# Kernel optimization log

Hardware: AMD Instinct MI355X
Metric: run time of the kernel (lower is better)

## Reference

```python
import jax, jax.numpy as jnp
import numpy as np

B, D, N_TYPES = 512, 768, 16
MARGIN = 1.0


def setup_inputs() -> dict:
    key = jax.random.key(0)
    k1, k2 = jax.random.split(key)
    entity_types = jax.random.randint(k1, (B,), 0, N_TYPES, dtype=jnp.int64)
    embeddings = jax.random.normal(k2, (B, D), dtype=jnp.float32)
    return {"entity_types": entity_types, "embeddings": embeddings}


def _pairwise_l2(x):
    # Euclidean distance matrix [B, B], matching torch.cdist(x, x, p=2)
    sq_norm = jnp.sum(x * x, axis=-1)  # [B]
    sq = sq_norm[:, None] + sq_norm[None, :] - 2.0 * (x @ x.T)
    sq = jnp.maximum(sq, 0.0)
    # safe sqrt: zero gradient where sq == 0 (diagonal)
    return jnp.where(sq > 0, jnp.sqrt(jnp.where(sq > 0, sq, 1.0)), 0.0)


def reference(entity_types, embeddings):
    # type_coherence[i, j] = (type_i == type_j)
    type_coherence = entity_types[:, None] == entity_types[None, :]  # [B, B]
    # valid_triplets[a, p, n] = same_type(a, p) & different_type(a, n)
    valid_triplets = type_coherence[:, :, None] & (~type_coherence)[:, None, :]  # [B, B, B]
    distances = _pairwise_l2(embeddings)  # [B, B]
    # triplet_distances[a, p, n] = (d[a, p] - d[a, n]) masked by validity
    triplet_distances = (distances[:, :, None] - distances[:, None, :]) * valid_triplets
    # NOTE: faithful to original — margin added to ALL B^3 entries before clamp,
    # so each invalid triplet contributes clamp(margin, 0) = margin to the sum.
    loss = jnp.sum(jnp.maximum(triplet_distances + MARGIN, 0.0))
    return loss / jnp.sum(valid_triplets)
```

## Files before the change

kernel.cpp:

```cpp
#include <hip/hip_runtime.h>

#define BSZ 512
#define DIM 768
#define KSPLIT 4
#define KSEG (DIM / KSPLIT)
#define KT 32
#define NCHK (KSEG / KT)
#define TILE 64
#define NTYPES 16
#define MARGIN 1.0f

__global__ __launch_bounds__(256) void dot_partial_kernel(
    const float* __restrict__ emb,
    float* __restrict__ part,
    float* __restrict__ ndiag,
    double* __restrict__ accum)
{
    const int tid = threadIdx.x;
    const int tx = tid & 15, ty = tid >> 4;
    const int blk = blockIdx.x;
    const int ks = blk >> 6;
    const int tile = blk & 63;
    const int ti = tile >> 3, tj = tile & 7;
    const int i0 = ti * TILE, j0 = tj * TILE;

    if (blk == 0 && tid == 0) *accum = 0.0;

    __shared__ float sA[2][KT][TILE + 4];
    __shared__ float sB[2][KT][TILE + 4];

    const int srow = tid >> 2;
    const int g = tid & 3;
    const float* gA = emb + (size_t)(i0 + srow) * DIM + ks * KSEG;
    const float* gB = emb + (size_t)(j0 + srow) * DIM + ks * KSEG;

    float4 a0 = *(const float4*)(gA + 4 * g);
    float4 a1 = *(const float4*)(gA + 4 * (g + 4));
    float4 b0 = *(const float4*)(gB + 4 * g);
    float4 b1 = *(const float4*)(gB + 4 * (g + 4));

    {
        float (*pA)[TILE + 4] = sA[0];
        float (*pB)[TILE + 4] = sB[0];
        pA[4*g+0][srow]=a0.x; pA[4*g+1][srow]=a0.y; pA[4*g+2][srow]=a0.z; pA[4*g+3][srow]=a0.w;
        pA[4*(g+4)+0][srow]=a1.x; pA[4*(g+4)+1][srow]=a1.y; pA[4*(g+4)+2][srow]=a1.z; pA[4*(g+4)+3][srow]=a1.w;
        pB[4*g+0][srow]=b0.x; pB[4*g+1][srow]=b0.y; pB[4*g+2][srow]=b0.z; pB[4*g+3][srow]=b0.w;
        pB[4*(g+4)+0][srow]=b1.x; pB[4*(g+4)+1][srow]=b1.y; pB[4*(g+4)+2][srow]=b1.z; pB[4*(g+4)+3][srow]=b1.w;
    }
    __syncthreads();

    float acc[4][4] = {};

    for (int c = 0; c < NCHK; ++c) {
        const int cur = c & 1;
        float4 qa0, qa1, qb0, qb1;
        if (c + 1 < NCHK) {
            const float* pa = gA + (c + 1) * KT;
            const float* pb = gB + (c + 1) * KT;
            qa0 = *(const float4*)(pa + 4 * g);
            qa1 = *(const float4*)(pa + 4 * (g + 4));
            qb0 = *(const float4*)(pb + 4 * g);
            qb1 = *(const float4*)(pb + 4 * (g + 4));
        }
        #pragma unroll
        for (int k = 0; k < KT; ++k) {
            float4 av = *(const float4*)&sA[cur][k][4 * ty];
            float4 bv = *(const float4*)&sB[cur][k][4 * tx];
            acc[0][0] = fmaf(av.x, bv.x, acc[0][0]);
            acc[0][1] = fmaf(av.x, bv.y, acc[0][1]);
            acc[0][2] = fmaf(av.x, bv.z, acc[0][2]);
            acc[0][3] = fmaf(av.x, bv.w, acc[0][3]);
            acc[1][0] = fmaf(av.y, bv.x, acc[1][0]);
            acc[1][1] = fmaf(av.y, bv.y, acc[1][1]);
            acc[1][2] = fmaf(av.y, bv.z, acc[1][2]);
            acc[1][3] = fmaf(av.y, bv.w, acc[1][3]);
            acc[2][0] = fmaf(av.z, bv.x, acc[2][0]);
            acc[2][1] = fmaf(av.z, bv.y, acc[2][1]);
            acc[2][2] = fmaf(av.z, bv.z, acc[2][2]);
            acc[2][3] = fmaf(av.z, bv.w, acc[2][3]);
            acc[3][0] = fmaf(av.w, bv.x, acc[3][0]);
            acc[3][1] = fmaf(av.w, bv.y, acc[3][1]);
            acc[3][2] = fmaf(av.w, bv.z, acc[3][2]);
            acc[3][3] = fmaf(av.w, bv.w, acc[3][3]);
        }
        if (c + 1 < NCHK) {
            float (*pA)[TILE + 4] = sA[1 - cur];
            float (*pB)[TILE + 4] = sB[1 - cur];
            pA[4*g+0][srow]=qa0.x; pA[4*g+1][srow]=qa0.y; pA[4*g+2][srow]=qa0.z; pA[4*g+3][srow]=qa0.w;
            pA[4*(g+4)+0][srow]=qa1.x; pA[4*(g+4)+1][srow]=qa1.y; pA[4*(g+4)+2][srow]=qa1.z; pA[4*(g+4)+3][srow]=qa1.w;
            pB[4*g+0][srow]=qb0.x; pB[4*g+1][srow]=qb0.y; pB[4*g+2][srow]=qb0.z; pB[4*g+3][srow]=qb0.w;
            pB[4*(g+4)+0][srow]=qb1.x; pB[4*(g+4)+1][srow]=qb1.y; pB[4*(g+4)+2][srow]=qb1.z; pB[4*(g+4)+3][srow]=qb1.w;
        }
        __syncthreads();
    }

    float* pbuf = part + (size_t)ks * BSZ * BSZ;
    #pragma unroll
    for (int r = 0; r < 4; ++r) {
        const int gi = i0 + 4 * ty + r;
        float4 v = make_float4(acc[r][0], acc[r][1], acc[r][2], acc[r][3]);
        *(float4*)&pbuf[(size_t)gi * BSZ + j0 + 4 * tx] = v;
    }
    if (ti == tj && tx == ty) {
        #pragma unroll
        for (int r = 0; r < 4; ++r)
            ndiag[ks * BSZ + i0 + 4 * ty + r] = acc[r][r];
    }
}

__global__ __launch_bounds__(256) void triplet_kernel(
    const float* __restrict__ part, const float* __restrict__ ndiag,
    const int* __restrict__ types, double* __restrict__ accum)
{
    const int a = blockIdx.x;
    const int tid = threadIdx.x;
    const int lane = tid & 63;
    __shared__ float nrm[BSZ];
    __shared__ float pos[BSZ], neg[BSZ];
    __shared__ int npos, nneg;
    __shared__ float wsum[4];
    if (tid == 0) { npos = 0; nneg = 0; }
    for (int j = tid; j < BSZ; j += 256)
        nrm[j] = ndiag[j] + ndiag[BSZ + j] + ndiag[2 * BSZ + j] + ndiag[3 * BSZ + j];
    const int ta = types[a];
    __syncthreads();

    const float na = nrm[a];
    const size_t rb = (size_t)a * BSZ;
    const size_t PS = (size_t)BSZ * BSZ;

    for (int j = tid; j < BSZ; j += 256) {
        const float sp = part[rb + j] + part[PS + rb + j]
                       + part[2 * PS + rb + j] + part[3 * PS + rb + j];
        const float d = sqrtf(fmaxf(na + nrm[j] - 2.f * sp, 0.f));
        const bool isp = (types[j] == ta);
        const unsigned long long m = __ballot(isp);
        const unsigned long long below = m & ((1ull << lane) - 1ull);
        const int cp = __popcll(m);
        int basep = 0, basen = 0;
        if (lane == 0) {
            basep = atomicAdd(&npos, cp);
            basen = atomicAdd(&nneg, 64 - cp);
        }
        basep = __shfl(basep, 0);
        basen = __shfl(basen, 0);
        const int pbelow = (int)__popcll(below);
        if (isp) pos[basep + pbelow] = d;
        else     neg[basen + (lane - pbelow)] = d;
    }
    __syncthreads();
    const int np = npos, nn = nneg;

    float local = 0.f;
    for (int pi = 0; pi < np; ++pi) {
        const float dpm = pos[pi] + MARGIN;
        for (int n = tid; n < nn; n += 256)
            local += fmaxf(dpm - neg[n], 0.f);
    }

    #pragma unroll
    for (int off = 32; off > 0; off >>= 1) local += __shfl_down(local, off);
    if (lane == 0) wsum[tid >> 6] = local;
    __syncthreads();
    if (tid == 0) {
        double s = (double)wsum[0] + (double)wsum[1] + (double)wsum[2] + (double)wsum[3];
        atomicAdd(accum, s);
    }
}

__global__ void finalize_kernel(const int* __restrict__ types,
                                const double* __restrict__ accum,
                                float* __restrict__ out) {
    __shared__ int cnt[NTYPES];
    if (threadIdx.x < NTYPES) cnt[threadIdx.x] = 0;
    __syncthreads();
    for (int i = threadIdx.x; i < BSZ; i += blockDim.x) atomicAdd(&cnt[types[i]], 1);
    __syncthreads();
    if (threadIdx.x == 0) {
        long long V = 0;
        for (int t = 0; t < NTYPES; t++) {
            long long c = cnt[t];
            V += c * c * (long long)(BSZ - c);
        }
        const long long B3 = (long long)BSZ * BSZ * BSZ;
        double total = *accum + (double)(B3 - V) * (double)MARGIN;
        out[0] = (float)(total / (double)V);
    }
}

extern "C" void kernel_launch(void* const* d_in, const int* in_sizes, int n_in,
                              void* d_out, int out_size, void* d_ws, size_t ws_size,
                              hipStream_t stream) {
    const int* types = (const int*)d_in[0];
    const float* emb = (const float*)d_in[1];
    float* out = (float*)d_out;

    float* part = (float*)d_ws;
    float* ndiag = part + (size_t)KSPLIT * BSZ * BSZ;
    double* accum = (double*)(ndiag + KSPLIT * BSZ);

    dot_partial_kernel<<<256, 256, 0, stream>>>(emb, part, ndiag, accum);
    triplet_kernel<<<BSZ, 256, 0, stream>>>(part, ndiag, types, accum);
    finalize_kernel<<<1, 256, 0, stream>>>(types, accum, out);
}
```

Baseline: 80.33 us.

## Fuse GEMM, triplet and finalize kernels into one persistent kernel with grid barrier

Merges the three launches into a single 256-block kernel. A spin-wait atomic grid barrier separates the partial-dot GEMM phase from the triplet phase, and each block now handles two anchors. A last-block-done counter runs the finalize step in place of a separate kernel. This removes two launch gaps but adds a memset, halves the parallelism in the triplet phase, and relies on all 256 blocks being co-resident for the barrier.

```diff
diff --git a/kernel.cpp b/kernel.cpp
--- a/kernel.cpp
+++ b/kernel.cpp
@@ -9,12 +9,15 @@
 #define TILE 64
 #define NTYPES 16
 #define MARGIN 1.0f
-
-__global__ __launch_bounds__(256) void dot_partial_kernel(
-    const float* __restrict__ emb,
+#define NBLK 256
+
+__global__ __launch_bounds__(256) void fused_kernel(
+    const float* __restrict__ emb, const int* __restrict__ types,
     float* __restrict__ part,
     float* __restrict__ ndiag,
-    double* __restrict__ accum)
+    double* __restrict__ accum,
+    unsigned* __restrict__ ctrl,
+    float* __restrict__ out)
 {
     const int tid = threadIdx.x;
     const int tx = tid & 15, ty = tid >> 4;
@@ -24,167 +27,183 @@
     const int ti = tile >> 3, tj = tile & 7;
     const int i0 = ti * TILE, j0 = tj * TILE;
 
-    if (blk == 0 && tid == 0) *accum = 0.0;
-
     __shared__ float sA[2][KT][TILE + 4];
     __shared__ float sB[2][KT][TILE + 4];
-
-    const int srow = tid >> 2;
-    const int g = tid & 3;
-    const float* gA = emb + (size_t)(i0 + srow) * DIM + ks * KSEG;
-    const float* gB = emb + (size_t)(j0 + srow) * DIM + ks * KSEG;
-
-    float4 a0 = *(const float4*)(gA + 4 * g);
-    float4 a1 = *(const float4*)(gA + 4 * (g + 4));
-    float4 b0 = *(const float4*)(gB + 4 * g);
-    float4 b1 = *(const float4*)(gB + 4 * (g + 4));
-
-    {
-        float (*pA)[TILE + 4] = sA[0];
-        float (*pB)[TILE + 4] = sB[0];
-        pA[4*g+0][srow]=a0.x; pA[4*g+1][srow]=a0.y; pA[4*g+2][srow]=a0.z; pA[4*g+3][srow]=a0.w;
-        pA[4*(g+4)+0][srow]=a1.x; pA[4*(g+4)+1][srow]=a1.y; pA[4*(g+4)+2][srow]=a1.z; pA[4*(g+4)+3][srow]=a1.w;
-        pB[4*g+0][srow]=b0.x; pB[4*g+1][srow]=b0.y; pB[4*g+2][srow]=b0.z; pB[4*g+3][srow]=b0.w;
-        pB[4*(g+4)+0][srow]=b1.x; pB[4*(g+4)+1][srow]=b1.y; pB[4*(g+4)+2][srow]=b1.z; pB[4*(g+4)+3][srow]=b1.w;
-    }
-    __syncthreads();
-
-    float acc[4][4] = {};
-
-    for (int c = 0; c < NCHK; ++c) {
-        const int cur = c & 1;
-        float4 qa0, qa1, qb0, qb1;
-        if (c + 1 < NCHK) {
-            const float* pa = gA + (c + 1) * KT;
-            const float* pb = gB + (c + 1) * KT;
-            qa0 = *(const float4*)(pa + 4 * g);
-            qa1 = *(const float4*)(pa + 4 * (g + 4));
-            qb0 = *(const float4*)(pb + 4 * g);
-            qb1 = *(const float4*)(pb + 4 * (g + 4));
-        }
-        #pragma unroll
-        for (int k = 0; k < KT; ++k) {
-            float4 av = *(const float4*)&sA[cur][k][4 * ty];
-            float4 bv = *(const float4*)&sB[cur][k][4 * tx];
-            acc[0][0] = fmaf(av.x, bv.x, acc[0][0]);
-            acc[0][1] = fmaf(av.x, bv.y, acc[0][1]);
-            acc[0][2] = fmaf(av.x, bv.z, acc[0][2]);
-            acc[0][3] = fmaf(av.x, bv.w, acc[0][3]);
-            acc[1][0] = fmaf(av.y, bv.x, acc[1][0]);
-            acc[1][1] = fmaf(av.y, bv.y, acc[1][1]);
-            acc[1][2] = fmaf(av.y, bv.z, acc[1][2]);
-            acc[1][3] = fmaf(av.y, bv.w, acc[1][3]);
-            acc[2][0] = fmaf(av.z, bv.x, acc[2][0]);
-            acc[2][1] = fmaf(av.z, bv.y, acc[2][1]);
-            acc[2][2] = fmaf(av.z, bv.z, acc[2][2]);
-            acc[2][3] = fmaf(av.z, bv.w, acc[2][3]);
-            acc[3][0] = fmaf(av.w, bv.x, acc[3][0]);
-            acc[3][1] = fmaf(av.w, bv.y, acc[3][1]);
-            acc[3][2] = fmaf(av.w, bv.z, acc[3][2]);
-            acc[3][3] = fmaf(av.w, bv.w, acc[3][3]);
-        }
-        if (c + 1 < NCHK) {
-            float (*pA)[TILE + 4] = sA[1 - cur];
-            float (*pB)[TILE + 4] = sB[1 - cur];
-            pA[4*g+0][srow]=qa0.x; pA[4*g+1][srow]=qa0.y; pA[4*g+2][srow]=qa0.z; pA[4*g+3][srow]=qa0.w;
-            pA[4*(g+4)+0][srow]=qa1.x; pA[4*(g+4)+1][srow]=qa1.y; pA[4*(g+4)+2][srow]=qa1.z; pA[4*(g+4)+3][srow]=qa1.w;
-            pB[4*g+0][srow]=qb0.x; pB[4*g+1][srow]=qb0.y; pB[4*g+2][srow]=qb0.z; pB[4*g+3][srow]=qb0.w;
-            pB[4*(g+4)+0][srow]=qb1.x; pB[4*(g+4)+1][srow]=qb1.y; pB[4*(g+4)+2][srow]=qb1.z; pB[4*(g+4)+3][srow]=qb1.w;
-        }
-        __syncthreads();
-    }
-
-    float* pbuf = part + (size_t)ks * BSZ * BSZ;
-    #pragma unroll
-    for (int r = 0; r < 4; ++r) {
-        const int gi = i0 + 4 * ty + r;
-        float4 v = make_float4(acc[r][0], acc[r][1], acc[r][2], acc[r][3]);
-        *(float4*)&pbuf[(size_t)gi * BSZ + j0 + 4 * tx] = v;
-    }
-    if (ti == tj && tx == ty) {
-        #pragma unroll
-        for (int r = 0; r < 4; ++r)
-            ndiag[ks * BSZ + i0 + 4 * ty + r] = acc[r][r];
-    }
-}
-
-__global__ __launch_bounds__(256) void triplet_kernel(
-    const float* __restrict__ part, const float* __restrict__ ndiag,
-    const int* __restrict__ types, double* __restrict__ accum)
-{
-    const int a = blockIdx.x;
-    const int tid = threadIdx.x;
-    const int lane = tid & 63;
     __shared__ float nrm[BSZ];
     __shared__ float pos[BSZ], neg[BSZ];
     __shared__ int npos, nneg;
     __shared__ float wsum[4];
-    if (tid == 0) { npos = 0; nneg = 0; }
+    __shared__ int winner;
+    __shared__ int cnt[NTYPES];
+
+    {
+        const int srow = tid >> 2;
+        const int g = tid & 3;
+        const float* gA = emb + (size_t)(i0 + srow) * DIM + ks * KSEG;
+        const float* gB = emb + (size_t)(j0 + srow) * DIM + ks * KSEG;
+
+        float4 a0 = *(const float4*)(gA + 4 * g);
+        float4 a1 = *(const float4*)(gA + 4 * (g + 4));
+        float4 b0 = *(const float4*)(gB + 4 * g);
+        float4 b1 = *(const float4*)(gB + 4 * (g + 4));
+        {
+            float (*pA)[TILE + 4] = sA[0];
+            float (*pB)[TILE + 4] = sB[0];
+            pA[4*g+0][srow]=a0.x; pA[4*g+1][srow]=a0.y; pA[4*g+2][srow]=a0.z; pA[4*g+3][srow]=a0.w;
+            pA[4*(g+4)+0][srow]=a1.x; pA[4*(g+4)+1][srow]=a1.y; pA[4*(g+4)+2][srow]=a1.z; pA[4*(g+4)+3][srow]=a1.w;
+            pB[4*g+0][srow]=b0.x; pB[4*g+1][srow]=b0.y; pB[4*g+2][srow]=b0.z; pB[4*g+3][srow]=b0.w;
+            pB[4*(g+4)+0][srow]=b1.x; pB[4*(g+4)+1][srow]=b1.y; pB[4*(g+4)+2][srow]=b1.z; pB[4*(g+4)+3][srow]=b1.w;
+        }
+        __syncthreads();
+
+        float acc[4][4] = {};
+        for (int c = 0; c < NCHK; ++c) {
+            const int cur = c & 1;
+            float4 qa0, qa1, qb0, qb1;
+            if (c + 1 < NCHK) {
+                const float* pa = gA + (c + 1) * KT;
+                const float* pb = gB + (c + 1) * KT;
+                qa0 = *(const float4*)(pa + 4 * g);
+                qa1 = *(const float4*)(pa + 4 * (g + 4));
+                qb0 = *(const float4*)(pb + 4 * g);
+                qb1 = *(const float4*)(pb + 4 * (g + 4));
+            }
+            #pragma unroll
+            for (int k = 0; k < KT; ++k) {
+                float4 av = *(const float4*)&sA[cur][k][4 * ty];
+                float4 bv = *(const float4*)&sB[cur][k][4 * tx];
+                acc[0][0] = fmaf(av.x, bv.x, acc[0][0]);
+                acc[0][1] = fmaf(av.x, bv.y, acc[0][1]);
+                acc[0][2] = fmaf(av.x, bv.z, acc[0][2]);
+                acc[0][3] = fmaf(av.x, bv.w, acc[0][3]);
+                acc[1][0] = fmaf(av.y, bv.x, acc[1][0]);
+                acc[1][1] = fmaf(av.y, bv.y, acc[1][1]);
+                acc[1][2] = fmaf(av.y, bv.z, acc[1][2]);
+                acc[1][3] = fmaf(av.y, bv.w, acc[1][3]);
+                acc[2][0] = fmaf(av.z, bv.x, acc[2][0]);
+                acc[2][1] = fmaf(av.z, bv.y, acc[2][1]);
+                acc[2][2] = fmaf(av.z, bv.z, acc[2][2]);
+                acc[2][3] = fmaf(av.z, bv.w, acc[2][3]);
+                acc[3][0] = fmaf(av.w, bv.x, acc[3][0]);
+                acc[3][1] = fmaf(av.w, bv.y, acc[3][1]);
+                acc[3][2] = fmaf(av.w, bv.z, acc[3][2]);
+                acc[3][3] = fmaf(av.w, bv.w, acc[3][3]);
+            }
+            if (c + 1 < NCHK) {
+                float (*pA)[TILE + 4] = sA[1 - cur];
+                float (*pB)[TILE + 4] = sB[1 - cur];
+                pA[4*g+0][srow]=qa0.x; pA[4*g+1][srow]=qa0.y; pA[4*g+2][srow]=qa0.z; pA[4*g+3][srow]=qa0.w;
+                pA[4*(g+4)+0][srow]=qa1.x; pA[4*(g+4)+1][srow]=qa1.y; pA[4*(g+4)+2][srow]=qa1.z; pA[4*(g+4)+3][srow]=qa1.w;
+                pB[4*g+0][srow]=qb0.x; pB[4*g+1][srow]=qb0.y; pB[4*g+2][srow]=qb0.z; pB[4*g+3][srow]=qb0.w;
+                pB[4*(g+4)+0][srow]=qb1.x; pB[4*(g+4)+1][srow]=qb1.y; pB[4*(g+4)+2][srow]=qb1.z; pB[4*(g+4)+3][srow]=qb1.w;
+            }
+            __syncthreads();
+        }
+
+        float* pbuf = part + (size_t)ks * BSZ * BSZ;
+        #pragma unroll
+        for (int r = 0; r < 4; ++r) {
+            const int gi = i0 + 4 * ty + r;
+            float4 v = make_float4(acc[r][0], acc[r][1], acc[r][2], acc[r][3]);
+            *(float4*)&pbuf[(size_t)gi * BSZ + j0 + 4 * tx] = v;
+        }
+        if (ti == tj && tx == ty) {
+            #pragma unroll
+            for (int r = 0; r < 4; ++r)
+                ndiag[ks * BSZ + i0 + 4 * ty + r] = acc[r][r];
+        }
+    }
+
+    __syncthreads();
+    if (tid == 0) {
+        __hip_atomic_fetch_add(&ctrl[0], 1u, __ATOMIC_RELEASE,
+                               __HIP_MEMORY_SCOPE_AGENT);
+        while (__hip_atomic_load(&ctrl[0], __ATOMIC_RELAXED,
+                                 __HIP_MEMORY_SCOPE_AGENT) < NBLK)
+            __builtin_amdgcn_s_sleep(2);
+        (void)__hip_atomic_load(&ctrl[0], __ATOMIC_ACQUIRE,
+                                __HIP_MEMORY_SCOPE_AGENT);
+    }
+    __syncthreads();
+
+    const int lane = tid & 63;
     for (int j = tid; j < BSZ; j += 256)
         nrm[j] = ndiag[j] + ndiag[BSZ + j] + ndiag[2 * BSZ + j] + ndiag[3 * BSZ + j];
-    const int ta = types[a];
-    __syncthreads();
-
-    const float na = nrm[a];
-    const size_t rb = (size_t)a * BSZ;
+    __syncthreads();
+
     const size_t PS = (size_t)BSZ * BSZ;
-
-    for (int j = tid; j < BSZ; j += 256) {
-        const float sp = part[rb + j] + part[PS + rb + j]
-                       + part[2 * PS + rb + j] + part[3 * PS + rb + j];
-        const float d = sqrtf(fmaxf(na + nrm[j] - 2.f * sp, 0.f));
-        const bool isp = (types[j] == ta);
-        const unsigned long long m = __ballot(isp);
-        const unsigned long long below = m & ((1ull << lane) - 1ull);
-        const int cp = __popcll(m);
-        int basep = 0, basen = 0;
-        if (lane == 0) {
-            basep = atomicAdd(&npos, cp);
-            basen = atomicAdd(&nneg, 64 - cp);
-        }
-        basep = __shfl(basep, 0);
-        basen = __shfl(basen, 0);
-        const int pbelow = (int)__popcll(below);
-        if (isp) pos[basep + pbelow] = d;
-        else     neg[basen + (lane - pbelow)] = d;
-    }
-    __syncthreads();
-    const int np = npos, nn = nneg;
-
-    float local = 0.f;
-    for (int pi = 0; pi < np; ++pi) {
-        const float dpm = pos[pi] + MARGIN;
-        for (int n = tid; n < nn; n += 256)
-            local += fmaxf(dpm - neg[n], 0.f);
-    }
-
-    #pragma unroll
-    for (int off = 32; off > 0; off >>= 1) local += __shfl_down(local, off);
-    if (lane == 0) wsum[tid >> 6] = local;
-    __syncthreads();
+    double blocksum = 0.0;
+    for (int ai = 0; ai < 2; ++ai) {
+        const int a = blk * 2 + ai;
+        if (tid == 0) { npos = 0; nneg = 0; }
+        const int ta = types[a];
+        const float na = nrm[a];
+        const size_t rb = (size_t)a * BSZ;
+        __syncthreads();
+
+        for (int j = tid; j < BSZ; j += 256) {
+            const float sp = part[rb + j] + part[PS + rb + j]
+                           + part[2 * PS + rb + j] + part[3 * PS + rb + j];
+            const float d = sqrtf(fmaxf(na + nrm[j] - 2.f * sp, 0.f));
+            const bool isp = (types[j] == ta);
+            const unsigned long long m = __ballot(isp);
+            const unsigned long long below = m & ((1ull << lane) - 1ull);
+            const int cp = __popcll(m);
+            int basep = 0, basen = 0;
+            if (lane == 0) {
+                basep = atomicAdd(&npos, cp);
+                basen = atomicAdd(&nneg, 64 - cp);
+            }
+            basep = __shfl(basep, 0);
+            basen = __shfl(basen, 0);
+            const int pbelow = (int)__popcll(below);
+            if (isp) pos[basep + pbelow] = d;
+            else     neg[basen + (lane - pbelow)] = d;
+        }
+        __syncthreads();
+        const int np = npos, nn = nneg;
+
+        float local = 0.f;
+        for (int pi = 0; pi < np; ++pi) {
+            const float dpm = pos[pi] + MARGIN;
+            for (int n = tid; n < nn; n += 256)
+                local += fmaxf(dpm - neg[n], 0.f);
+        }
+
+        #pragma unroll
+        for (int off = 32; off > 0; off >>= 1) local += __shfl_down(local, off);
+        if (lane == 0) wsum[tid >> 6] = local;
+        __syncthreads();
+        if (tid == 0)
+            blocksum += (double)wsum[0] + (double)wsum[1]
+                      + (double)wsum[2] + (double)wsum[3];
+        __syncthreads();
+    }
+    if (tid == 0) atomicAdd(accum, blocksum);
+
     if (tid == 0) {
-        double s = (double)wsum[0] + (double)wsum[1] + (double)wsum[2] + (double)wsum[3];
-        atomicAdd(accum, s);
-    }
-}
-
-__global__ void finalize_kernel(const int* __restrict__ types,
-                                const double* __restrict__ accum,
-                                float* __restrict__ out) {
-    __shared__ int cnt[NTYPES];
-    if (threadIdx.x < NTYPES) cnt[threadIdx.x] = 0;
-    __syncthreads();
-    for (int i = threadIdx.x; i < BSZ; i += blockDim.x) atomicAdd(&cnt[types[i]], 1);
-    __syncthreads();
-    if (threadIdx.x == 0) {
-        long long V = 0;
-        for (int t = 0; t < NTYPES; t++) {
-            long long c = cnt[t];
-            V += c * c * (long long)(BSZ - c);
-        }
-        const long long B3 = (long long)BSZ * BSZ * BSZ;
-        double total = *accum + (double)(B3 - V) * (double)MARGIN;
-        out[0] = (float)(total / (double)V);
+        unsigned t = __hip_atomic_fetch_add(&ctrl[1], 1u, __ATOMIC_ACQ_REL,
+                                            __HIP_MEMORY_SCOPE_AGENT);
+        winner = (t == NBLK - 1) ? 1 : 0;
+    }
+    __syncthreads();
+    if (winner) {
+        if (tid < NTYPES) cnt[tid] = 0;
+        __syncthreads();
+        for (int i = tid; i < BSZ; i += 256) atomicAdd(&cnt[types[i]], 1);
+        __syncthreads();
+        if (tid == 0) {
+            long long V = 0;
+            for (int t2 = 0; t2 < NTYPES; t2++) {
+                long long c = cnt[t2];
+                V += c * c * (long long)(BSZ - c);
+            }
+            const long long B3 = (long long)BSZ * BSZ * BSZ;
+            double total = __hip_atomic_load(accum, __ATOMIC_ACQUIRE,
+                                             __HIP_MEMORY_SCOPE_AGENT)
+                         + (double)(B3 - V) * (double)MARGIN;
+            out[0] = (float)(total / (double)V);
+        }
     }
 }
 
@@ -197,9 +216,11 @@
 
     float* part = (float*)d_ws;
     float* ndiag = part + (size_t)KSPLIT * BSZ * BSZ;
-    double* accum = (double*)(ndiag + KSPLIT * BSZ);
-
-    dot_partial_kernel<<<256, 256, 0, stream>>>(emb, part, ndiag, accum);
-    triplet_kernel<<<BSZ, 256, 0, stream>>>(part, ndiag, types, accum);
-    finalize_kernel<<<1, 256, 0, stream>>>(types, accum, out);
+    char* tail = (char*)(ndiag + KSPLIT * BSZ);
+    double* accum = (double*)tail;
+    unsigned* ctrl = (unsigned*)(tail + 8);
+
+    hipMemsetAsync(tail, 0, 16, stream);
+    fused_kernel<<<NBLK, 256, 0, stream>>>(emb, types, part, ndiag,
+                                           accum, ctrl, out);
 }
```

Measured after the change: 103.8 us. +29.2%, slower.
